# Kernel optimization log

Hardware: AMD Instinct MI355X
Metric: run time of the kernel (lower is better)

The kernel has to match this reference:

```python
import jax, jax.numpy as jnp
import numpy as np

BETA = 1.0
TARGET_ENTROPY = 0.0
EPS = 1e-8


def setup_inputs() -> dict:
    key = jax.random.key(0)
    k1, k2 = jax.random.split(key)
    B, S, H, K = 4, 2048, 1024, 10
    hidden_states = jax.random.normal(k1, (B, S, H), dtype=jnp.float32)
    kernel_centers = jax.random.normal(k2, (K, H), dtype=jnp.float32) * 0.1
    kernel_weights = jnp.ones((K,), dtype=jnp.float32) / K
    kernel_scales = jnp.ones((K,), dtype=jnp.float32)  # kernel_bandwidth = 1.0
    return {
        "hidden_states": hidden_states,
        "kernel_centers": kernel_centers,
        "kernel_weights": kernel_weights,
        "kernel_scales": kernel_scales,
    }


def _knife_entropy(x, centers, weights, scales):
    # x: [N, H], centers: [K, H].  Gram-matrix form of sum_h (x-c)^2:
    x_sq = jnp.sum(x * x, axis=1, keepdims=True)          # [N, 1]
    c_sq = jnp.sum(centers * centers, axis=1)[None, :]    # [1, K]
    dist_sq = jnp.maximum(x_sq + c_sq - 2.0 * (x @ centers.T), 0.0)  # [N, K]
    kernel_vals = jnp.exp(-dist_sq / (2.0 * scales[None, :] ** 2))   # [N, K]
    density = kernel_vals @ weights                       # [N]
    return -jnp.mean(jnp.log(density + EPS))


def reference(hidden_states, kernel_centers, kernel_weights, kernel_scales):
    H = hidden_states.shape[-1]
    h_flat = hidden_states.reshape(-1, H)                 # [B*S, H]
    h_entropy = _knife_entropy(h_flat, kernel_centers, kernel_weights, kernel_scales)
    entropy_loss = BETA * h_entropy
    target_entropy_loss = (h_entropy - TARGET_ENTROPY) ** 2  # mse vs scalar target
    total_loss = entropy_loss + target_entropy_loss
    # order: entropy_loss, target_entropy_loss, total_loss, h_entropy
    return jnp.stack([entropy_loss, target_entropy_loss, total_loss, h_entropy])
```

## Files before the change

kernel.cpp:

```cpp
#include <hip/hip_runtime.h>
#include <math.h>

#define N_ROWS 8192
#define HDIM   1024
#define KK     10
#define EPSF   1e-8f

__global__ __launch_bounds__(256, 2)
void knife_main(const float* __restrict__ x,
                const float* __restrict__ centers,
                const float* __restrict__ weights,
                const float* __restrict__ scales,
                float* __restrict__ partials) {
    const int lane = threadIdx.x & 63;
    const int wave_in_block = threadIdx.x >> 6;
    const int gwave = blockIdx.x * 4 + wave_in_block;
    const int nwaves = gridDim.x * 4;

    const float4* c4 = (const float4*)centers;
    float4 c[KK][4];
#pragma unroll
    for (int k = 0; k < KK; ++k) {
#pragma unroll
        for (int j = 0; j < 4; ++j) {
            c[k][j] = c4[k * (HDIM / 4) + lane + 64 * j];
        }
    }

    float csq[KK];
#pragma unroll
    for (int k = 0; k < KK; ++k) {
        float s = 0.f;
#pragma unroll
        for (int j = 0; j < 4; ++j) {
            float4 v = c[k][j];
            s += v.x * v.x + v.y * v.y + v.z * v.z + v.w * v.w;
        }
#pragma unroll
        for (int off = 32; off > 0; off >>= 1) s += __shfl_xor(s, off, 64);
        csq[k] = s;
    }

    float w[KK], inv2s2[KK];
#pragma unroll
    for (int k = 0; k < KK; ++k) {
        w[k] = weights[k];
        float sc = scales[k];
        inv2s2[k] = 1.0f / (2.0f * sc * sc);
    }

    float logsum = 0.f;
    for (int row = gwave; row < N_ROWS; row += nwaves) {
        const float4* xr = (const float4*)(x + (size_t)row * HDIM);
        float4 xv[4];
#pragma unroll
        for (int j = 0; j < 4; ++j) xv[j] = xr[lane + 64 * j];

        float acc[KK + 1];
#pragma unroll
        for (int k = 0; k <= KK; ++k) acc[k] = 0.f;
#pragma unroll
        for (int j = 0; j < 4; ++j) {
            float4 v = xv[j];
            acc[KK] += v.x * v.x + v.y * v.y + v.z * v.z + v.w * v.w;
#pragma unroll
            for (int k = 0; k < KK; ++k) {
                float4 cv = c[k][j];
                acc[k] += v.x * cv.x + v.y * cv.y + v.z * cv.z + v.w * cv.w;
            }
        }
#pragma unroll
        for (int k = 0; k <= KK; ++k) {
            float s = acc[k];
#pragma unroll
            for (int off = 32; off > 0; off >>= 1) s += __shfl_xor(s, off, 64);
            acc[k] = s;
        }
        float density = 0.f;
#pragma unroll
        for (int k = 0; k < KK; ++k) {
            float d = acc[KK] + csq[k] - 2.0f * acc[k];
            d = fmaxf(d, 0.0f);
            density += w[k] * __expf(-d * inv2s2[k]);
        }
        logsum += __logf(density + EPSF);
    }

    __shared__ float red[4];
    if (lane == 0) red[wave_in_block] = logsum;
    __syncthreads();
    if (threadIdx.x == 0) {
        partials[blockIdx.x] = red[0] + red[1] + red[2] + red[3];
    }
}

__global__ __launch_bounds__(256)
void knife_final(const float* __restrict__ partials, float* __restrict__ out) {
    __shared__ float red[4];
    int t = threadIdx.x;
    float s = partials[t] + partials[t + 256];
#pragma unroll
    for (int off = 32; off > 0; off >>= 1) s += __shfl_xor(s, off, 64);
    if ((t & 63) == 0) red[t >> 6] = s;
    __syncthreads();
    if (t == 0) {
        float total = red[0] + red[1] + red[2] + red[3];
        float h = -total / (float)N_ROWS;
        out[0] = h;
        out[1] = h * h;
        out[2] = h + h * h;
        out[3] = h;
    }
}

extern "C" void kernel_launch(void* const* d_in, const int* in_sizes, int n_in,
                              void* d_out, int out_size, void* d_ws, size_t ws_size,
                              hipStream_t stream) {
    const float* x       = (const float*)d_in[0];
    const float* centers = (const float*)d_in[1];
    const float* weights = (const float*)d_in[2];
    const float* scales  = (const float*)d_in[3];
    float* out      = (float*)d_out;
    float* partials = (float*)d_ws;

    knife_main<<<512, 256, 0, stream>>>(x, centers, weights, scales, partials);
    knife_final<<<1, 256, 0, stream>>>(partials, out);
}
```

Before: 89.01 us.

## Use DPP wave reductions and prefetch next row in fully unrolled loop

Swaps the shuffle-based butterfly reductions for DPP row operations with a final readlane, so each of the 11 per-row reductions costs fewer instructions and no LDS-backed shuffles. The row loop is fully unrolled to 4 iterations, a fixed count derived from 8192 rows over 2048 waves, and each iteration issues the next row's loads before computing the current one so memory latency overlaps with compute. This hardcodes the grid and row count and raises register pressure from the extra prefetch buffer.

```diff
diff --git a/kernel.cpp b/kernel.cpp
--- a/kernel.cpp
+++ b/kernel.cpp
@@ -6,6 +6,20 @@
 #define KK     10
 #define EPSF   1e-8f
 
+#define DPP_ADD(x, ctrl, rmask, bmask)                                        \
+    x += __int_as_float(__builtin_amdgcn_update_dpp(                          \
+        0, __float_as_int(x), ctrl, rmask, bmask, true))
+
+__device__ __forceinline__ float wave_allreduce_add(float x) {
+    DPP_ADD(x, 0x111, 0xf, 0xf);
+    DPP_ADD(x, 0x112, 0xf, 0xf);
+    DPP_ADD(x, 0x114, 0xf, 0xe);
+    DPP_ADD(x, 0x118, 0xf, 0xc);
+    DPP_ADD(x, 0x142, 0xa, 0xf);
+    DPP_ADD(x, 0x143, 0xc, 0xf);
+    return __int_as_float(__builtin_amdgcn_readlane(__float_as_int(x), 63));
+}
+
 __global__ __launch_bounds__(256, 2)
 void knife_main(const float* __restrict__ x,
                 const float* __restrict__ centers,
@@ -13,19 +27,18 @@
                 const float* __restrict__ scales,
                 float* __restrict__ partials) {
     const int lane = threadIdx.x & 63;
-    const int wave_in_block = threadIdx.x >> 6;
-    const int gwave = blockIdx.x * 4 + wave_in_block;
+    const int wid  = threadIdx.x >> 6;
+    const int gwave  = blockIdx.x * 4 + wid;
     const int nwaves = gridDim.x * 4;
+    const int ROWS   = N_ROWS / 2048;
 
     const float4* c4 = (const float4*)centers;
     float4 c[KK][4];
 #pragma unroll
-    for (int k = 0; k < KK; ++k) {
+    for (int k = 0; k < KK; ++k)
 #pragma unroll
-        for (int j = 0; j < 4; ++j) {
+        for (int j = 0; j < 4; ++j)
             c[k][j] = c4[k * (HDIM / 4) + lane + 64 * j];
-        }
-    }
 
     float csq[KK];
 #pragma unroll
@@ -36,9 +49,7 @@
             float4 v = c[k][j];
             s += v.x * v.x + v.y * v.y + v.z * v.z + v.w * v.w;
         }
-#pragma unroll
-        for (int off = 32; off > 0; off >>= 1) s += __shfl_xor(s, off, 64);
-        csq[k] = s;
+        csq[k] = wave_allreduce_add(s);
     }
 
     float w[KK], inv2s2[KK];
@@ -49,12 +60,23 @@
         inv2s2[k] = 1.0f / (2.0f * sc * sc);
     }
 
+    const float4* x4 = (const float4*)x;
     float logsum = 0.f;
-    for (int row = gwave; row < N_ROWS; row += nwaves) {
-        const float4* xr = (const float4*)(x + (size_t)row * HDIM);
-        float4 xv[4];
+
+    int row = gwave;
+    float4 xv[4], nx[4];
 #pragma unroll
-        for (int j = 0; j < 4; ++j) xv[j] = xr[lane + 64 * j];
+    for (int j = 0; j < 4; ++j)
+        xv[j] = x4[((size_t)row << 8) + lane + 64 * j];
+
+#pragma unroll
+    for (int i = 0; i < 4; ++i) {
+        const int nrow = row + nwaves;
+        if (i + 1 < ROWS) {
+#pragma unroll
+            for (int j = 0; j < 4; ++j)
+                nx[j] = x4[((size_t)nrow << 8) + lane + 64 * j];
+        }
 
         float acc[KK + 1];
 #pragma unroll
@@ -69,29 +91,27 @@
                 acc[k] += v.x * cv.x + v.y * cv.y + v.z * cv.z + v.w * cv.w;
             }
         }
-#pragma unroll
-        for (int k = 0; k <= KK; ++k) {
-            float s = acc[k];
-#pragma unroll
-            for (int off = 32; off > 0; off >>= 1) s += __shfl_xor(s, off, 64);
-            acc[k] = s;
-        }
+
+        float xsq = wave_allreduce_add(acc[KK]);
         float density = 0.f;
 #pragma unroll
         for (int k = 0; k < KK; ++k) {
-            float d = acc[KK] + csq[k] - 2.0f * acc[k];
-            d = fmaxf(d, 0.0f);
+            float dot = wave_allreduce_add(acc[k]);
+            float d = fmaxf(xsq + csq[k] - 2.0f * dot, 0.0f);
             density += w[k] * __expf(-d * inv2s2[k]);
         }
         logsum += __logf(density + EPSF);
+
+#pragma unroll
+        for (int j = 0; j < 4; ++j) xv[j] = nx[j];
+        row = nrow;
     }
 
     __shared__ float red[4];
-    if (lane == 0) red[wave_in_block] = logsum;
+    if (lane == 0) red[wid] = logsum;
     __syncthreads();
-    if (threadIdx.x == 0) {
+    if (threadIdx.x == 0)
         partials[blockIdx.x] = red[0] + red[1] + red[2] + red[3];
-    }
 }
 
 __global__ __launch_bounds__(256)
@@ -99,8 +119,7 @@
     __shared__ float red[4];
     int t = threadIdx.x;
     float s = partials[t] + partials[t + 256];
-#pragma unroll
-    for (int off = 32; off > 0; off >>= 1) s += __shfl_xor(s, off, 64);
+    s = wave_allreduce_add(s);
     if ((t & 63) == 0) red[t >> 6] = s;
     __syncthreads();
     if (t == 0) {
```

Result: faster. 86.98 us (-2.3%).
